# Optimization experiments

Hardware: AMD Instinct MI355X
Metric: run time of the kernel (lower is better)

The kernel has to match this reference:

```python
import jax, jax.numpy as jnp
import numpy as np
from jax.ops import segment_sum

N_NODES = 100000
N_EDGES = 3200000
IN_DIM = 128
HID = 128
INT_DIM = 512
OUT_DIM = 3


def gcn_conv(x, W, b, src, dst, n):
    # PyG GCNConv (eval): add self-loops, symmetric normalization, aggregate, bias.
    loop = jnp.arange(n, dtype=src.dtype)
    s = jnp.concatenate([src, loop])
    d = jnp.concatenate([dst, loop])
    deg = segment_sum(jnp.ones_like(d, dtype=x.dtype), d, num_segments=n)  # [N]
    dinv = jnp.where(deg > 0, jax.lax.rsqrt(jnp.maximum(deg, 1e-12)), 0.0)
    norm = dinv[s] * dinv[d]                      # [E+N]
    h = x @ W                                      # [N, F_out]
    msg = h[s] * norm[:, None]                    # gather + scale
    return segment_sum(msg, d, num_segments=n) + b


def setup_inputs() -> dict:
    key = jax.random.key(0)
    ks = jax.random.split(key, 12)
    def lin(kw, kb, fi, fo):
        lim = 1.0 / np.sqrt(fi)
        W = jax.random.uniform(kw, (fi, fo), jnp.float32, -lim, lim)
        b = jax.random.uniform(kb, (fo,), jnp.float32, -lim, lim)
        return W, b
    x = jax.random.normal(ks[0], (N_NODES, IN_DIM), jnp.float32)
    edge_index = jax.random.randint(ks[1], (2, N_EDGES), 0, N_NODES, dtype=jnp.int64)
    W1, b1 = lin(ks[2], ks[3], IN_DIM, HID)
    W2, b2 = lin(ks[4], ks[5], HID, HID)
    W3, b3 = lin(ks[6], ks[7], HID, INT_DIM)
    Wi, bi = lin(ks[8], ks[9], INT_DIM, INT_DIM)
    Wc, bc = lin(ks[10], ks[11], INT_DIM, OUT_DIM)
    return {"x": x, "edge_index": edge_index, "W1": W1, "b1": b1, "W2": W2,
            "b2": b2, "W3": W3, "b3": b3, "Wi": Wi, "bi": bi, "Wc": Wc, "bc": bc}


def reference(x, edge_index, W1, b1, W2, b2, W3, b3, Wi, bi, Wc, bc):
    src, dst = edge_index[0], edge_index[1]
    n = x.shape[0]
    h = jax.nn.relu(gcn_conv(x, W1, b1, src, dst, n))
    h = jax.nn.relu(gcn_conv(h, W2, b2, src, dst, n))
    h = jax.nn.relu(gcn_conv(h, W3, b3, src, dst, n))
    h = jax.nn.relu(h @ Wi + bi)
    return h @ Wc + bc
```

## Files before the change

### kernel.cpp

```cpp
#include <hip/hip_runtime.h>
#include <hip/hip_fp16.h>

#define NN 100000
#define NE 3200000
#define NB 391
#define NBLK 512
#define EPB 6250

typedef unsigned int uint32;
typedef unsigned short u16;
typedef long long ll64;
typedef __attribute__((ext_vector_type(8))) _Float16 half8;
typedef __attribute__((ext_vector_type(4))) float f32x4;

__device__ inline float2 h2f2(uint32 u) {
  __half2 h = *reinterpret_cast<__half2*>(&u);
  return __half22float2(h);
}
__device__ inline uint32 f2h2(float x, float y) {
  return (uint32)__half_as_ushort(__float2half(x)) |
         ((uint32)__half_as_ushort(__float2half(y)) << 16);
}
__device__ inline int edge_at(const void* ei, int is64, ll64 idx) {
  return is64 ? (int)((const ll64*)ei)[idx] : ((const int*)ei)[idx];
}

__global__ void k_probe(const int* __restrict__ ei, int* __restrict__ flag) {
  if (threadIdx.x == 0) {
    int acc = 0;
#pragma unroll
    for (int i = 1; i < 32; i += 2) acc |= ei[i];
    *flag = (acc == 0) ? 1 : 0;
  }
}

__global__ __launch_bounds__(256) void k_binB(const void* __restrict__ ei,
                                              const int* __restrict__ flag,
                                              int* __restrict__ tbl) {
  __shared__ int h[NB];
  int k = blockIdx.x, tid = threadIdx.x;
  for (int i = tid; i < NB; i += 256) h[i] = 0;
  __syncthreads();
  int is64 = *flag;
  ll64 beg = (ll64)k * EPB, end = beg + EPB;
  for (ll64 i = beg + tid; i < end; i += 256)
    atomicAdd(&h[edge_at(ei, is64, (ll64)NE + i) >> 8], 1);
  __syncthreads();
  for (int i = tid; i < NB; i += 256) tbl[k * NB + i] = h[i];
}
__global__ __launch_bounds__(512) void k_binC1(int* __restrict__ tbl,
                                               int* __restrict__ total) {
  __shared__ int sd[NBLK];
  int b = blockIdx.x, tid = threadIdx.x;
  int v = tbl[tid * NB + b];
  sd[tid] = v;
  __syncthreads();
  for (int off = 1; off < NBLK; off <<= 1) {
    int t = (tid >= off) ? sd[tid - off] : 0;
    __syncthreads();
    sd[tid] += t;
    __syncthreads();
  }
  tbl[tid * NB + b] = sd[tid] - v;
  if (tid == NBLK - 1) total[b] = sd[NBLK - 1];
}
__global__ __launch_bounds__(512) void k_binC2(const int* __restrict__ total,
                                               int* __restrict__ bbase,
                                               int* __restrict__ offs) {
  __shared__ int sd[512];
  int tid = threadIdx.x;
  int v = (tid < NB) ? total[tid] : 0;
  sd[tid] = v;
  __syncthreads();
  for (int off = 1; off < 512; off <<= 1) {
    int t = (tid >= off) ? sd[tid - off] : 0;
    __syncthreads();
    sd[tid] += t;
    __syncthreads();
  }
  if (tid < NB) bbase[tid] = sd[tid] - v;
  if (tid == 0) offs[NN] = NE;
}
__global__ __launch_bounds__(256) void k_binD(const void* __restrict__ ei,
                                              const int* __restrict__ flag,
                                              const int* __restrict__ tbl,
                                              const int* __restrict__ bbase,
                                              uint32* __restrict__ binned) {
  __shared__ int lb[NB];
  __shared__ int lc[NB];
  int k = blockIdx.x, tid = threadIdx.x;
  for (int i = tid; i < NB; i += 256) {
    lb[i] = tbl[k * NB + i] + bbase[i];
    lc[i] = 0;
  }
  __syncthreads();
  int is64 = *flag;
  ll64 beg = (ll64)k * EPB, end = beg + EPB;
  for (ll64 i = beg + tid; i < end; i += 256) {
    int s = edge_at(ei, is64, i);
    int d = edge_at(ei, is64, (ll64)NE + i);
    int b = d >> 8;
    int r = atomicAdd(&lc[b], 1);
    binned[lb[b] + r] = (uint32)s | ((uint32)(d & 255) << 24);
  }
}
__global__ __launch_bounds__(256) void k_binE(const uint32* __restrict__ binned,
                                              const int* __restrict__ bbase,
                                              const int* __restrict__ total,
                                              int* __restrict__ offs,
                                              float* __restrict__ dinv,
                                              int* __restrict__ csr) {
  __shared__ int cnt[256], pref[256], fil[256];
  int b = blockIdx.x, tid = threadIdx.x;
  cnt[tid] = 0;
  fil[tid] = 0;
  __syncthreads();
  int base = bbase[b], tot = total[b];
  for (int i = tid; i < tot; i += 256) atomicAdd(&cnt[binned[base + i] >> 24], 1);
  __syncthreads();
  int v = cnt[tid];
  pref[tid] = v;
  __syncthreads();
  for (int off = 1; off < 256; off <<= 1) {
    int t = (tid >= off) ? pref[tid - off] : 0;
    __syncthreads();
    pref[tid] += t;
    __syncthreads();
  }
  int myoff = pref[tid] - v;
  pref[tid] = myoff;
  int node = b * 256 + tid;
  if (node < NN) {
    offs[node] = base + myoff;
    dinv[node] = rsqrtf((float)(v + 1));
  }
  __syncthreads();
  for (int i = tid; i < tot; i += 256) {
    uint32 w = binned[base + i];
    int dl = w >> 24;
    int r = atomicAdd(&fil[dl], 1);
    csr[base + pref[dl] + r] = (int)(w & 0xFFFFFFu);
  }
}

__device__ inline void packOne(const float* __restrict__ W, u16* __restrict__ ph,
                               int K, int N, int t) {
  int j = t & 7, lane = (t >> 3) & 63, tl = t >> 9;
  int kbn = K >> 5;
  int kb = tl % kbn, ntile = tl / kbn;
  int k = kb * 32 + (lane >> 4) * 8 + j;
  int n2 = ntile * 16 + (lane & 15);
  ph[t] = __half_as_ushort(__float2half(W[k * N + n2]));
}
__global__ void k_packAll(const float* W1, const float* W2, const float* W3,
                          const float* Wi, u16* p1, u16* p2, u16* p3, u16* pi) {
  int t = blockIdx.x * blockDim.x + threadIdx.x;
  if (t < 16384) packOne(W1, p1, 128, 128, t);
  else if (t < 32768) packOne(W2, p2, 128, 128, t - 16384);
  else if (t < 98304) packOne(W3, p3, 128, 512, t - 32768);
  else if (t < 360448) packOne(Wi, pi, 512, 512, t - 98304);
}

__global__ void k_half(const float4* __restrict__ x, ushort4* __restrict__ xh, int n4) {
  int i = blockIdx.x * blockDim.x + threadIdx.x;
  if (i < n4) {
    float4 v = x[i];
    ushort4 o;
    o.x = __half_as_ushort(__float2half(v.x));
    o.y = __half_as_ushort(__float2half(v.y));
    o.z = __half_as_ushort(__float2half(v.z));
    o.w = __half_as_ushort(__float2half(v.w));
    xh[i] = o;
  }
}

__global__ void k_agg(const uint32* __restrict__ xi, uint32* __restrict__ o,
                      const int* __restrict__ csr, const int* __restrict__ offs,
                      const float* __restrict__ dinv, int n) {
  int node = blockIdx.x * 4 + (threadIdx.x >> 6);
  int lane = threadIdx.x & 63;
  if (node >= n) return;
  int beg = offs[node], end = offs[node + 1];
  float ax = 0.f, ay = 0.f;
  int j = beg;
  for (; j + 3 < end; j += 4) {
    int s0 = csr[j], s1 = csr[j + 1], s2 = csr[j + 2], s3 = csr[j + 3];
    float d0 = dinv[s0], d1 = dinv[s1], d2 = dinv[s2], d3 = dinv[s3];
    float2 r0 = h2f2(xi[(ll64)s0 * 64 + lane]);
    float2 r1 = h2f2(xi[(ll64)s1 * 64 + lane]);
    float2 r2 = h2f2(xi[(ll64)s2 * 64 + lane]);
    float2 r3 = h2f2(xi[(ll64)s3 * 64 + lane]);
    ax += d0 * r0.x + d1 * r1.x + d2 * r2.x + d3 * r3.x;
    ay += d0 * r0.y + d1 * r1.y + d2 * r2.y + d3 * r3.y;
  }
  for (; j < end; j++) {
    int s = csr[j];
    float d = dinv[s];
    float2 r = h2f2(xi[(ll64)s * 64 + lane]);
    ax += d * r.x;
    ay += d * r.y;
  }
  float di = dinv[node];
  float2 sf = h2f2(xi[(ll64)node * 64 + lane]);
  float vx = di * (ax + di * sf.x);
  float vy = di * (ay + di * sf.y);
  o[(ll64)node * 64 + lane] = f2h2(vx, vy);
}

__global__ __launch_bounds__(256, 4) void k_gemm_mfma(
    const u16* __restrict__ A, const u16* __restrict__ Bp,
    const float* __restrict__ bias, u16* __restrict__ Co, int M, int N, int K) {
  int wave = threadIdx.x >> 6, lane = threadIdx.x & 63;
  int quad = lane >> 4, l16 = lane & 15;
  int row0 = blockIdx.x * 64, col0 = blockIdx.y * 64;
  int m = row0 + wave * 16 + l16;
  int mc = (m < M) ? m : (M - 1);
  int kbn = K >> 5;
  f32x4 acc[4] = {{0,0,0,0},{0,0,0,0},{0,0,0,0},{0,0,0,0}};
  const half8* Ar = (const half8*)&A[(ll64)mc * K];
  half8 ac = Ar[quad];
  half8 an = ac;
  half8 bc_[4], bn_[4];
#pragma unroll
  for (int nt = 0; nt < 4; nt++)
    bc_[nt] = *(const half8*)&Bp[((ll64)(((col0 >> 4) + nt) * kbn) * 64 + lane) * 8];
  for (int kb = 0; kb < kbn; kb++) {
    int kn = kb + 1;
    if (kn < kbn) {
      an = Ar[kn * 4 + quad];
#pragma unroll
      for (int nt = 0; nt < 4; nt++)
        bn_[nt] = *(const half8*)&Bp[((ll64)(((col0 >> 4) + nt) * kbn + kn) * 64 + lane) * 8];
    }
#pragma unroll
    for (int nt = 0; nt < 4; nt++)
      acc[nt] = __builtin_amdgcn_mfma_f32_16x16x32_f16(ac, bc_[nt], acc[nt], 0, 0, 0);
    ac = an;
#pragma unroll
    for (int nt = 0; nt < 4; nt++) bc_[nt] = bn_[nt];
  }
#pragma unroll
  for (int nt = 0; nt < 4; nt++) {
    int cc = col0 + nt * 16 + l16;
    float bv = bias[cc];
#pragma unroll
    for (int r = 0; r < 4; r++) {
      int rr = row0 + wave * 16 + quad * 4 + r;
      if (rr < M)
        Co[(ll64)rr * N + cc] =
            __half_as_ushort(__float2half(fmaxf(acc[nt][r] + bv, 0.0f)));
    }
  }
}

__global__ __launch_bounds__(256, 4) void k_tail32(
    const u16* __restrict__ a3, const u16* __restrict__ W3p,
    const float* __restrict__ b3, const u16* __restrict__ Wip,
    const float* __restrict__ bi, const float* __restrict__ Wc,
    const float* __restrict__ bc, float* __restrict__ out, int M) {
  __shared__ u16 h3s[32 * 512];
  __shared__ float sRed[4][32][3];
  int tid = threadIdx.x;
  int wave = tid >> 6, lane = tid & 63, quad = lane >> 4, l16 = lane & 15;
  int row0 = blockIdx.x * 32;

  half8 af[2][4];
#pragma unroll
  for (int rt = 0; rt < 2; rt++) {
    const half8* Ar = (const half8*)&a3[(ll64)(row0 + rt * 16 + l16) * 128];
#pragma unroll
    for (int kb = 0; kb < 4; kb++) af[rt][kb] = Ar[kb * 4 + quad];
  }
  {
    f32x4 acc0 = {0, 0, 0, 0}, acc1 = {0, 0, 0, 0};
    half8 bcur = *(const half8*)&W3p[((ll64)(wave * 32) * 64 + lane) * 8];
    half8 bnxt = bcur;
    for (int t = 0; t < 32; t++) {
      if (t + 1 < 32)
        bnxt = *(const half8*)&W3p[((ll64)(wave * 32 + t + 1) * 64 + lane) * 8];
      int kb = t & 3;
      acc0 = __builtin_amdgcn_mfma_f32_16x16x32_f16(af[0][kb], bcur, acc0, 0, 0, 0);
      acc1 = __builtin_amdgcn_mfma_f32_16x16x32_f16(af[1][kb], bcur, acc1, 0, 0, 0);
      if (kb == 3) {
        int nt = wave * 8 + (t >> 2);
        int col = nt * 16 + l16;
        float bv = b3[col];
#pragma unroll
        for (int r = 0; r < 4; r++) {
          int row0l = quad * 4 + r;
          float v0 = fmaxf(acc0[r] + bv, 0.0f);
          float v1 = fmaxf(acc1[r] + bv, 0.0f);
          int oct0 = (col >> 3) ^ (row0l & 7);
          h3s[row0l * 512 + oct0 * 8 + (col & 7)] = __half_as_ushort(__float2half(v0));
          int row1l = 16 + row0l;
          int oct1 = (col >> 3) ^ (row1l & 7);
          h3s[row1l * 512 + oct1 * 8 + (col & 7)] = __half_as_ushort(__float2half(v1));
        }
        acc0 = (f32x4){0, 0, 0, 0};
        acc1 = (f32x4){0, 0, 0, 0};
      }
      bcur = bnxt;
    }
  }
  __syncthreads();

  float acc3[2][4][3] = {};
  {
    f32x4 acc0 = {0, 0, 0, 0}, acc1 = {0, 0, 0, 0};
    half8 bcur = *(const half8*)&Wip[((ll64)(wave * 128) * 64 + lane) * 8];
    half8 bnxt = bcur;
    int r0l = l16, r1l = 16 + l16;
    int sw0 = r0l & 7;
    for (int t = 0; t < 128; t++) {
      if (t + 1 < 128)
        bnxt = *(const half8*)&Wip[((ll64)(wave * 128 + t + 1) * 64 + lane) * 8];
      int kb = t & 15;
      int oct = ((kb * 4 + quad) ^ sw0);
      half8 a0 = *(const half8*)&h3s[r0l * 512 + oct * 8];
      half8 a1 = *(const half8*)&h3s[r1l * 512 + oct * 8];
      acc0 = __builtin_amdgcn_mfma_f32_16x16x32_f16(a0, bcur, acc0, 0, 0, 0);
      acc1 = __builtin_amdgcn_mfma_f32_16x16x32_f16(a1, bcur, acc1, 0, 0, 0);
      if (kb == 15) {
        int nt = wave * 8 + (t >> 4);
        int col = nt * 16 + l16;
        float bv = bi[col];
        float w0 = Wc[col * 3 + 0], w1 = Wc[col * 3 + 1], w2 = Wc[col * 3 + 2];
#pragma unroll
        for (int r = 0; r < 4; r++) {
          float v0 = fmaxf(acc0[r] + bv, 0.0f);
          float v1 = fmaxf(acc1[r] + bv, 0.0f);
          acc3[0][r][0] += v0 * w0; acc3[0][r][1] += v0 * w1; acc3[0][r][2] += v0 * w2;
          acc3[1][r][0] += v1 * w0; acc3[1][r][1] += v1 * w1; acc3[1][r][2] += v1 * w2;
        }
        acc0 = (f32x4){0, 0, 0, 0};
        acc1 = (f32x4){0, 0, 0, 0};
      }
      bcur = bnxt;
    }
  }
#pragma unroll
  for (int rt = 0; rt < 2; rt++)
#pragma unroll
    for (int r = 0; r < 4; r++)
#pragma unroll
      for (int c = 0; c < 3; c++) {
        float v = acc3[rt][r][c];
        v += __shfl_xor(v, 1);
        v += __shfl_xor(v, 2);
        v += __shfl_xor(v, 4);
        v += __shfl_xor(v, 8);
        acc3[rt][r][c] = v;
      }
  if (l16 == 0) {
#pragma unroll
    for (int rt = 0; rt < 2; rt++)
#pragma unroll
      for (int r = 0; r < 4; r++)
#pragma unroll
        for (int c = 0; c < 3; c++)
          sRed[wave][rt * 16 + quad * 4 + r][c] = acc3[rt][r][c];
  }
  __syncthreads();
  if (tid < 96) {
    int row = tid / 3, c = tid % 3;
    out[(ll64)(row0 + row) * 3 + c] = sRed[0][row][c] + sRed[1][row][c] +
                                      sRed[2][row][c] + sRed[3][row][c] + bc[c];
  }
}

extern "C" void kernel_launch(void* const* d_in, const int* in_sizes, int n_in,
                              void* d_out, int out_size, void* d_ws, size_t ws_size,
                              hipStream_t stream) {
  const float* x  = (const float*)d_in[0];
  const void*  ei = d_in[1];
  const float* W1 = (const float*)d_in[2];
  const float* b1 = (const float*)d_in[3];
  const float* W2 = (const float*)d_in[4];
  const float* b2 = (const float*)d_in[5];
  const float* W3 = (const float*)d_in[6];
  const float* b3 = (const float*)d_in[7];
  const float* Wi = (const float*)d_in[8];
  const float* bi = (const float*)d_in[9];
  const float* Wc = (const float*)d_in[10];
  const float* bc = (const float*)d_in[11];
  float* out = (float*)d_out;

  char* ws = (char*)d_ws;
  const ll64 KB = 1ll << 10, MB = 1ll << 20;
  float* dinv  = (float*)(ws + 0);
  int*   offs  = (int*)(ws + 512 * KB);
  int*   flag  = (int*)(ws + 1 * MB);
  int*   total = (int*)(ws + 1 * MB + 64 * KB);
  int*   bbase = (int*)(ws + 1 * MB + 128 * KB);
  int*   tbl   = (int*)(ws + 1 * MB + 192 * KB);
  uint32* binned = (uint32*)(ws + 2 * MB);
  int*   csr   = (int*)(ws + 15 * MB);
  u16* pW1 = (u16*)(ws + 28 * MB);
  u16* pW2 = (u16*)(ws + 28 * MB + 64 * KB);
  u16* pW3 = (u16*)(ws + 28 * MB + 128 * KB);
  u16* pWi = (u16*)(ws + 28 * MB + 512 * KB);
  u16* xh   = (u16*)(ws + 29 * MB);
  u16* bufA = (u16*)(ws + 55 * MB);
  u16* bufB = (u16*)(ws + 81 * MB);

  const int TB = 256;
  k_probe<<<1, 64, 0, stream>>>((const int*)ei, flag);
  k_binB<<<NBLK, TB, 0, stream>>>(ei, flag, tbl);
  k_binC1<<<NB, NBLK, 0, stream>>>(tbl, total);
  k_binC2<<<1, 512, 0, stream>>>(total, bbase, offs);
  k_binD<<<NBLK, TB, 0, stream>>>(ei, flag, tbl, bbase, binned);
  k_binE<<<NB, TB, 0, stream>>>(binned, bbase, total, offs, dinv, csr);
  k_packAll<<<1408, TB, 0, stream>>>(W1, W2, W3, Wi, pW1, pW2, pW3, pWi);
  k_half<<<(NN * 32 + TB - 1) / TB, TB, 0, stream>>>((const float4*)x,
                                                     (ushort4*)xh, NN * 32);

  const int MBk = (NN + 63) / 64;
  int aggBlocks = (NN + 3) / 4;
  dim3 g128(MBk, 2);

  k_agg<<<aggBlocks, TB, 0, stream>>>((const uint32*)xh, (uint32*)bufA, csr, offs, dinv, NN);
  k_gemm_mfma<<<g128, TB, 0, stream>>>(bufA, pW1, b1, bufB, NN, 128, 128);
  k_agg<<<aggBlocks, TB, 0, stream>>>((const uint32*)bufB, (uint32*)bufA, csr, offs, dinv, NN);
  k_gemm_mfma<<<g128, TB, 0, stream>>>(bufA, pW2, b2, bufB, NN, 128, 128);
  k_agg<<<aggBlocks, TB, 0, stream>>>((const uint32*)bufB, (uint32*)bufA, csr, offs, dinv, NN);
  k_tail32<<<NN / 32, TB, 0, stream>>>(bufA, pW3, b3, pWi, bi, Wc, bc, out, NN);
}
```

Before: 752.1 us.

## Fold probe into binning kernels, merge pack/half, unroll agg, widen tail tile

The separate edge-dtype probe kernel goes away; each binning block now detects int64 indices itself. The weight-pack and x-to-half kernels are merged into one launch. The aggregation loop is unrolled to 8 edges with loads grouped ahead of the FMAs, giving more memory-level parallelism. The fused tail kernel handles 48 rows per block instead of 32, reusing each weight fragment across three MFMA tiles, packs pairs of half stores through a shuffle, and reuses the h3s shared buffer for the reduction. The trade-off is higher register pressure (occupancy hint lowered to 3) and some redundant probe reads per block.

```diff
diff --git a/kernel.cpp b/kernel.cpp
--- a/kernel.cpp
+++ b/kernel.cpp
@@ -24,24 +24,22 @@
 __device__ inline int edge_at(const void* ei, int is64, ll64 idx) {
   return is64 ? (int)((const ll64*)ei)[idx] : ((const int*)ei)[idx];
 }
-
-__global__ void k_probe(const int* __restrict__ ei, int* __restrict__ flag) {
-  if (threadIdx.x == 0) {
-    int acc = 0;
-#pragma unroll
-    for (int i = 1; i < 32; i += 2) acc |= ei[i];
-    *flag = (acc == 0) ? 1 : 0;
-  }
+__device__ inline int detect64(const int* ei32) {
+  int acc = 0;
+#pragma unroll
+  for (int k = 1; k < 32; k += 2) acc |= ei32[k];
+  return (acc == 0) ? 1 : 0;
 }
 
 __global__ __launch_bounds__(256) void k_binB(const void* __restrict__ ei,
-                                              const int* __restrict__ flag,
                                               int* __restrict__ tbl) {
   __shared__ int h[NB];
+  __shared__ int sIs64;
   int k = blockIdx.x, tid = threadIdx.x;
   for (int i = tid; i < NB; i += 256) h[i] = 0;
-  __syncthreads();
-  int is64 = *flag;
+  if (tid == 0) sIs64 = detect64((const int*)ei);
+  __syncthreads();
+  int is64 = sIs64;
   ll64 beg = (ll64)k * EPB, end = beg + EPB;
   for (ll64 i = beg + tid; i < end; i += 256)
     atomicAdd(&h[edge_at(ei, is64, (ll64)NE + i) >> 8], 1);
@@ -82,19 +80,20 @@
   if (tid == 0) offs[NN] = NE;
 }
 __global__ __launch_bounds__(256) void k_binD(const void* __restrict__ ei,
-                                              const int* __restrict__ flag,
                                               const int* __restrict__ tbl,
                                               const int* __restrict__ bbase,
                                               uint32* __restrict__ binned) {
   __shared__ int lb[NB];
   __shared__ int lc[NB];
+  __shared__ int sIs64;
   int k = blockIdx.x, tid = threadIdx.x;
   for (int i = tid; i < NB; i += 256) {
     lb[i] = tbl[k * NB + i] + bbase[i];
     lc[i] = 0;
   }
-  __syncthreads();
-  int is64 = *flag;
+  if (tid == 0) sIs64 = detect64((const int*)ei);
+  __syncthreads();
+  int is64 = sIs64;
   ll64 beg = (ll64)k * EPB, end = beg + EPB;
   for (ll64 i = beg + tid; i < end; i += 256) {
     int s = edge_at(ei, is64, i);
@@ -152,25 +151,25 @@
   int n2 = ntile * 16 + (lane & 15);
   ph[t] = __half_as_ushort(__float2half(W[k * N + n2]));
 }
-__global__ void k_packAll(const float* W1, const float* W2, const float* W3,
-                          const float* Wi, u16* p1, u16* p2, u16* p3, u16* pi) {
+__global__ void k_packhalf(const float* W1, const float* W2, const float* W3,
+                           const float* Wi, u16* p1, u16* p2, u16* p3, u16* pi,
+                           const float4* __restrict__ x, ushort4* __restrict__ xh) {
   int t = blockIdx.x * blockDim.x + threadIdx.x;
   if (t < 16384) packOne(W1, p1, 128, 128, t);
   else if (t < 32768) packOne(W2, p2, 128, 128, t - 16384);
   else if (t < 98304) packOne(W3, p3, 128, 512, t - 32768);
   else if (t < 360448) packOne(Wi, pi, 512, 512, t - 98304);
-}
-
-__global__ void k_half(const float4* __restrict__ x, ushort4* __restrict__ xh, int n4) {
-  int i = blockIdx.x * blockDim.x + threadIdx.x;
-  if (i < n4) {
-    float4 v = x[i];
-    ushort4 o;
-    o.x = __half_as_ushort(__float2half(v.x));
-    o.y = __half_as_ushort(__float2half(v.y));
-    o.z = __half_as_ushort(__float2half(v.z));
-    o.w = __half_as_ushort(__float2half(v.w));
-    xh[i] = o;
+  else {
+    int i = t - 360448;
+    if (i < NN * 32) {
+      float4 v = x[i];
+      ushort4 o;
+      o.x = __half_as_ushort(__float2half(v.x));
+      o.y = __half_as_ushort(__float2half(v.y));
+      o.z = __half_as_ushort(__float2half(v.z));
+      o.w = __half_as_ushort(__float2half(v.w));
+      xh[i] = o;
+    }
   }
 }
 
@@ -183,15 +182,21 @@
   int beg = offs[node], end = offs[node + 1];
   float ax = 0.f, ay = 0.f;
   int j = beg;
-  for (; j + 3 < end; j += 4) {
-    int s0 = csr[j], s1 = csr[j + 1], s2 = csr[j + 2], s3 = csr[j + 3];
-    float d0 = dinv[s0], d1 = dinv[s1], d2 = dinv[s2], d3 = dinv[s3];
-    float2 r0 = h2f2(xi[(ll64)s0 * 64 + lane]);
-    float2 r1 = h2f2(xi[(ll64)s1 * 64 + lane]);
-    float2 r2 = h2f2(xi[(ll64)s2 * 64 + lane]);
-    float2 r3 = h2f2(xi[(ll64)s3 * 64 + lane]);
-    ax += d0 * r0.x + d1 * r1.x + d2 * r2.x + d3 * r3.x;
-    ay += d0 * r0.y + d1 * r1.y + d2 * r2.y + d3 * r3.y;
+  for (; j + 7 < end; j += 8) {
+    int s[8];
+    float dd[8];
+    float2 rr[8];
+#pragma unroll
+    for (int q = 0; q < 8; q++) s[q] = csr[j + q];
+#pragma unroll
+    for (int q = 0; q < 8; q++) dd[q] = dinv[s[q]];
+#pragma unroll
+    for (int q = 0; q < 8; q++) rr[q] = h2f2(xi[(ll64)s[q] * 64 + lane]);
+#pragma unroll
+    for (int q = 0; q < 8; q++) {
+      ax += dd[q] * rr[q].x;
+      ay += dd[q] * rr[q].y;
+    }
   }
   for (; j < end; j++) {
     int s = csr[j];
@@ -253,93 +258,102 @@
   }
 }
 
-__global__ __launch_bounds__(256, 4) void k_tail32(
+__global__ __launch_bounds__(256, 3) void k_tail48(
     const u16* __restrict__ a3, const u16* __restrict__ W3p,
     const float* __restrict__ b3, const u16* __restrict__ Wip,
     const float* __restrict__ bi, const float* __restrict__ Wc,
     const float* __restrict__ bc, float* __restrict__ out, int M) {
-  __shared__ u16 h3s[32 * 512];
-  __shared__ float sRed[4][32][3];
+  __shared__ u16 h3s[48 * 512];
+  float* sRed = (float*)h3s;
   int tid = threadIdx.x;
   int wave = tid >> 6, lane = tid & 63, quad = lane >> 4, l16 = lane & 15;
-  int row0 = blockIdx.x * 32;
-
-  half8 af[2][4];
-#pragma unroll
-  for (int rt = 0; rt < 2; rt++) {
-    const half8* Ar = (const half8*)&a3[(ll64)(row0 + rt * 16 + l16) * 128];
+  int row0 = blockIdx.x * 48;
+
+  half8 af[3][4];
+#pragma unroll
+  for (int rt = 0; rt < 3; rt++) {
+    int r = row0 + rt * 16 + l16;
+    int rc = (r < M) ? r : (M - 1);
+    const half8* Ar = (const half8*)&a3[(ll64)rc * 128];
 #pragma unroll
     for (int kb = 0; kb < 4; kb++) af[rt][kb] = Ar[kb * 4 + quad];
   }
   {
-    f32x4 acc0 = {0, 0, 0, 0}, acc1 = {0, 0, 0, 0};
+    f32x4 acc[3] = {{0,0,0,0},{0,0,0,0},{0,0,0,0}};
     half8 bcur = *(const half8*)&W3p[((ll64)(wave * 32) * 64 + lane) * 8];
     half8 bnxt = bcur;
     for (int t = 0; t < 32; t++) {
       if (t + 1 < 32)
         bnxt = *(const half8*)&W3p[((ll64)(wave * 32 + t + 1) * 64 + lane) * 8];
       int kb = t & 3;
-      acc0 = __builtin_amdgcn_mfma_f32_16x16x32_f16(af[0][kb], bcur, acc0, 0, 0, 0);
-      acc1 = __builtin_amdgcn_mfma_f32_16x16x32_f16(af[1][kb], bcur, acc1, 0, 0, 0);
+#pragma unroll
+      for (int rt = 0; rt < 3; rt++)
+        acc[rt] = __builtin_amdgcn_mfma_f32_16x16x32_f16(af[rt][kb], bcur, acc[rt], 0, 0, 0);
       if (kb == 3) {
         int nt = wave * 8 + (t >> 2);
         int col = nt * 16 + l16;
         float bv = b3[col];
 #pragma unroll
-        for (int r = 0; r < 4; r++) {
-          int row0l = quad * 4 + r;
-          float v0 = fmaxf(acc0[r] + bv, 0.0f);
-          float v1 = fmaxf(acc1[r] + bv, 0.0f);
-          int oct0 = (col >> 3) ^ (row0l & 7);
-          h3s[row0l * 512 + oct0 * 8 + (col & 7)] = __half_as_ushort(__float2half(v0));
-          int row1l = 16 + row0l;
-          int oct1 = (col >> 3) ^ (row1l & 7);
-          h3s[row1l * 512 + oct1 * 8 + (col & 7)] = __half_as_ushort(__float2half(v1));
-        }
-        acc0 = (f32x4){0, 0, 0, 0};
-        acc1 = (f32x4){0, 0, 0, 0};
+        for (int rt = 0; rt < 3; rt++)
+#pragma unroll
+          for (int r = 0; r < 4; r++) {
+            int row = rt * 16 + quad * 4 + r;
+            u16 h = __half_as_ushort(__float2half(fmaxf(acc[rt][r] + bv, 0.0f)));
+            u16 nb = (u16)__shfl_xor((int)h, 1);
+            if ((l16 & 1) == 0) {
+              int oct = (col >> 3) ^ (row & 7);
+              uint32 w = (uint32)h | ((uint32)nb << 16);
+              *(uint32*)&h3s[row * 512 + oct * 8 + (col & 7)] = w;
+            }
+          }
+        acc[0] = (f32x4){0,0,0,0};
+        acc[1] = (f32x4){0,0,0,0};
+        acc[2] = (f32x4){0,0,0,0};
       }
       bcur = bnxt;
     }
   }
   __syncthreads();
 
-  float acc3[2][4][3] = {};
+  float acc3[3][4][3] = {};
   {
-    f32x4 acc0 = {0, 0, 0, 0}, acc1 = {0, 0, 0, 0};
+    f32x4 acc[3] = {{0,0,0,0},{0,0,0,0},{0,0,0,0}};
     half8 bcur = *(const half8*)&Wip[((ll64)(wave * 128) * 64 + lane) * 8];
     half8 bnxt = bcur;
-    int r0l = l16, r1l = 16 + l16;
-    int sw0 = r0l & 7;
+    int sw = l16 & 7;
     for (int t = 0; t < 128; t++) {
       if (t + 1 < 128)
         bnxt = *(const half8*)&Wip[((ll64)(wave * 128 + t + 1) * 64 + lane) * 8];
       int kb = t & 15;
-      int oct = ((kb * 4 + quad) ^ sw0);
-      half8 a0 = *(const half8*)&h3s[r0l * 512 + oct * 8];
-      half8 a1 = *(const half8*)&h3s[r1l * 512 + oct * 8];
-      acc0 = __builtin_amdgcn_mfma_f32_16x16x32_f16(a0, bcur, acc0, 0, 0, 0);
-      acc1 = __builtin_amdgcn_mfma_f32_16x16x32_f16(a1, bcur, acc1, 0, 0, 0);
+      int oct = (kb * 4 + quad) ^ sw;
+      half8 a0 = *(const half8*)&h3s[(l16)      * 512 + oct * 8];
+      half8 a1 = *(const half8*)&h3s[(16 + l16) * 512 + oct * 8];
+      half8 a2 = *(const half8*)&h3s[(32 + l16) * 512 + oct * 8];
+      acc[0] = __builtin_amdgcn_mfma_f32_16x16x32_f16(a0, bcur, acc[0], 0, 0, 0);
+      acc[1] = __builtin_amdgcn_mfma_f32_16x16x32_f16(a1, bcur, acc[1], 0, 0, 0);
+      acc[2] = __builtin_amdgcn_mfma_f32_16x16x32_f16(a2, bcur, acc[2], 0, 0, 0);
       if (kb == 15) {
-        int nt = wave * 8 + (t >> 4);
-        int col = nt * 16 + l16;
+        int col = (wave * 8 + (t >> 4)) * 16 + l16;
         float bv = bi[col];
         float w0 = Wc[col * 3 + 0], w1 = Wc[col * 3 + 1], w2 = Wc[col * 3 + 2];
 #pragma unroll
-        for (int r = 0; r < 4; r++) {
-          float v0 = fmaxf(acc0[r] + bv, 0.0f);
-          float v1 = fmaxf(acc1[r] + bv, 0.0f);
-          acc3[0][r][0] += v0 * w0; acc3[0][r][1] += v0 * w1; acc3[0][r][2] += v0 * w2;
-          acc3[1][r][0] += v1 * w0; acc3[1][r][1] += v1 * w1; acc3[1][r][2] += v1 * w2;
-        }
-        acc0 = (f32x4){0, 0, 0, 0};
-        acc1 = (f32x4){0, 0, 0, 0};
+        for (int rt = 0; rt < 3; rt++)
+#pragma unroll
+          for (int r = 0; r < 4; r++) {
+            float v = fmaxf(acc[rt][r] + bv, 0.0f);
+            acc3[rt][r][0] += v * w0;
+            acc3[rt][r][1] += v * w1;
+            acc3[rt][r][2] += v * w2;
+          }
+        acc[0] = (f32x4){0,0,0,0};
+        acc[1] = (f32x4){0,0,0,0};
+        acc[2] = (f32x4){0,0,0,0};
       }
       bcur = bnxt;
     }
   }
 #pragma unroll
-  for (int rt = 0; rt < 2; rt++)
+  for (int rt = 0; rt < 3; rt++)
 #pragma unroll
     for (int r = 0; r < 4; r++)
 #pragma unroll
@@ -351,20 +365,24 @@
         v += __shfl_xor(v, 8);
         acc3[rt][r][c] = v;
       }
+  __syncthreads();
   if (l16 == 0) {
 #pragma unroll
-    for (int rt = 0; rt < 2; rt++)
+    for (int rt = 0; rt < 3; rt++)
 #pragma unroll
       for (int r = 0; r < 4; r++)
 #pragma unroll
         for (int c = 0; c < 3; c++)
-          sRed[wave][rt * 16 + quad * 4 + r][c] = acc3[rt][r][c];
-  }
-  __syncthreads();
-  if (tid < 96) {
+          sRed[(wave * 48 + rt * 16 + quad * 4 + r) * 3 + c] = acc3[rt][r][c];
+  }
+  __syncthreads();
+  if (tid < 144) {
     int row = tid / 3, c = tid % 3;
-    out[(ll64)(row0 + row) * 3 + c] = sRed[0][row][c] + sRed[1][row][c] +
-                                      sRed[2][row][c] + sRed[3][row][c] + bc[c];
+    int gr = row0 + row;
+    if (gr < M)
+      out[(ll64)gr * 3 + c] = sRed[(0 * 48 + row) * 3 + c] + sRed[(1 * 48 + row) * 3 + c] +
+                              sRed[(2 * 48 + row) * 3 + c] + sRed[(3 * 48 + row) * 3 + c] +
+                              bc[c];
   }
 }
 
@@ -389,7 +407,6 @@
   const ll64 KB = 1ll << 10, MB = 1ll << 20;
   float* dinv  = (float*)(ws + 0);
   int*   offs  = (int*)(ws + 512 * KB);
-  int*   flag  = (int*)(ws + 1 * MB);
   int*   total = (int*)(ws + 1 * MB + 64 * KB);
   int*   bbase = (int*)(ws + 1 * MB + 128 * KB);
   int*   tbl   = (int*)(ws + 1 * MB + 192 * KB);
@@ -404,15 +421,13 @@
   u16* bufB = (u16*)(ws + 81 * MB);
 
   const int TB = 256;
-  k_probe<<<1, 64, 0, stream>>>((const int*)ei, flag);
-  k_binB<<<NBLK, TB, 0, stream>>>(ei, flag, tbl);
+  k_binB<<<NBLK, TB, 0, stream>>>(ei, tbl);
   k_binC1<<<NB, NBLK, 0, stream>>>(tbl, total);
   k_binC2<<<1, 512, 0, stream>>>(total, bbase, offs);
-  k_binD<<<NBLK, TB, 0, stream>>>(ei, flag, tbl, bbase, binned);
+  k_binD<<<NBLK, TB, 0, stream>>>(ei, tbl, bbase, binned);
   k_binE<<<NB, TB, 0, stream>>>(binned, bbase, total, offs, dinv, csr);
-  k_packAll<<<1408, TB, 0, stream>>>(W1, W2, W3, Wi, pW1, pW2, pW3, pWi);
-  k_half<<<(NN * 32 + TB - 1) / TB, TB, 0, stream>>>((const float4*)x,
-                                                     (ushort4*)xh, NN * 32);
+  k_packhalf<<<(360448 + NN * 32 + TB - 1) / TB, TB, 0, stream>>>(
+      W1, W2, W3, Wi, pW1, pW2, pW3, pWi, (const float4*)x, (ushort4*)xh);
 
   const int MBk = (NN + 63) / 64;
   int aggBlocks = (NN + 3) / 4;
@@ -423,5 +438,5 @@
   k_agg<<<aggBlocks, TB, 0, stream>>>((const uint32*)bufB, (uint32*)bufA, csr, offs, dinv, NN);
   k_gemm_mfma<<<g128, TB, 0, stream>>>(bufA, pW2, b2, bufB, NN, 128, 128);
   k_agg<<<aggBlocks, TB, 0, stream>>>((const uint32*)bufB, (uint32*)bufA, csr, offs, dinv, NN);
-  k_tail32<<<NN / 32, TB, 0, stream>>>(bufA, pW3, b3, pWi, bi, Wc, bc, out, NN);
-}
+  k_tail48<<<(NN + 47) / 48, TB, 0, stream>>>(bufA, pW3, b3, pWi, bi, Wc, bc, out, NN);
+}
```

Measured after the change: 737.3 us. -2.0%, faster.
